# Performance work log

Measured on AMD Instinct MI355X. Metric: run time of the kernel, lower is better.

The kernel has to match this reference:

```python
import jax, jax.numpy as jnp
import numpy as np

HEADS = 16
TARGET_TOKENS = 128  # deterministic choice of image_tokens (original picks randomly from [729,128])


def _1d_sincos(embed_dim, pos):
    omega = np.arange(embed_dim // 2, dtype=np.float32)
    omega /= embed_dim / 2.0
    omega = 1.0 / 10000 ** omega
    out = np.einsum('m,d->md', pos.reshape(-1), omega)
    return np.concatenate([np.sin(out), np.cos(out)], axis=1)


def spatial_pos_embed(embed_dim, grid_size):
    d_sp = embed_dim // 4 * 3
    gh = np.arange(grid_size, dtype=np.float32)
    grid = np.stack(np.meshgrid(gh, gh), axis=0).reshape([2, 1, grid_size, grid_size])
    emb = np.concatenate([_1d_sincos(d_sp // 2, grid[0]), _1d_sincos(d_sp // 2, grid[1])], axis=1)
    emb = emb[np.newaxis]
    pad = np.zeros((1, emb.shape[1], embed_dim - d_sp), dtype=np.float32)
    return np.concatenate([pad, emb], axis=-1).reshape(1, grid_size * grid_size, embed_dim)


def setup_inputs() -> dict:
    key = jax.random.key(0)
    ks = jax.random.split(key, 4)
    B, P, C, H = 64, 729, 1152, 3584
    x = jax.random.normal(ks[0], (B, P, C), jnp.float32)
    w1 = jax.random.normal(ks[1], (C, H), jnp.float32) * (1.0 / np.sqrt(C))
    b1 = jnp.zeros((H,), jnp.float32)
    w2 = jax.random.normal(ks[2], (H, H), jnp.float32) * (1.0 / np.sqrt(H))
    b2 = jnp.zeros((H,), jnp.float32)
    spatial_pos = jnp.asarray(spatial_pos_embed(C, 27))
    return {'x': x, 'spatial_pos': spatial_pos, 'w1': w1, 'b1': b1,
            'w2': w2, 'b2': b2, 'local_num_frames': 1}


def _match_indices(metric, r):
    # ToMe bipartite soft matching: metric [B, T, d]
    metric = metric / jnp.linalg.norm(metric, axis=-1, keepdims=True)
    a, b = metric[:, ::2], metric[:, 1::2]
    scores = jnp.einsum('bic,bjc->bij', a, b)   # [B, Ta, Tb]
    node_max = scores.max(-1)
    node_idx = scores.argmax(-1)
    edge_idx = jnp.argsort(-node_max, axis=-1)
    unm_idx = edge_idx[:, r:]                    # kept src tokens
    src_idx = edge_idx[:, :r]                    # merged src tokens
    dst_idx = jnp.take_along_axis(node_idx, src_idx, axis=-1)
    return unm_idx, src_idx, dst_idx


def _merge_sum(x, unm_idx, src_idx, dst_idx):
    src, dst = x[:, ::2], x[:, 1::2]
    unm = jnp.take_along_axis(src, unm_idx[:, :, None], axis=1)
    sel = jnp.take_along_axis(src, src_idx[:, :, None], axis=1)
    dst = jax.vmap(lambda d, i, v: d.at[i].add(v))(dst, dst_idx, sel)
    return jnp.concatenate([unm, dst], axis=1)


def merge_tokens(x, target, heads):
    b, p, c = x.shape
    if p == target:
        return x
    rs, tmp = [], p
    while tmp != target:
        if tmp - target <= tmp // 2:
            rs.append(tmp - target)
            break
        rs.append(tmp // 2)
        tmp -= tmp // 2
    size = jnp.ones((b, p, 1), x.dtype)
    for r in rs:  # static schedule, e.g. [364, 182, 55]
        t = x.shape[1]
        metric = x.reshape(b, t, heads, c // heads).mean(2)
        idxs = _match_indices(metric, r)
        x = _merge_sum(x * size, *idxs)
        size = _merge_sum(size, *idxs)
        x = x / size
    return x


def reference(x, spatial_pos, w1, b1, w2, b2, local_num_frames):
    # is_image=True path
    x = x + spatial_pos
    x = merge_tokens(x, TARGET_TOKENS, HEADS)
    h = jax.nn.gelu(jnp.einsum('bpc,ch->bph', x, w1) + b1, approximate=False)
    return jnp.einsum('bph,ho->bpo', h, w2) + b2
```

## Files before the change

kernel.cpp:

```cpp
#include <hip/hip_runtime.h>
#include <hip/hip_bf16.h>
#include <stdint.h>

#define BB 64
#define P0 729
#define CC 1152
#define HD 72
#define NHEAD 16
#define HH 3584
#define TT 128
#define NSTR 365
#define SCB 384
#define MAXCB 6

typedef __hip_bfloat16 bf16;
typedef unsigned short u16;
typedef __attribute__((ext_vector_type(8))) short short8;
typedef __attribute__((ext_vector_type(4))) float floatx4;

__device__ inline u16 f2bf(float v) {
  bf16 h = __float2bfloat16(v);
  return *(u16*)&h;
}

__device__ inline void load_lds16(const void* g, void* l) {
  __builtin_amdgcn_global_load_lds(
      (const __attribute__((address_space(1))) uint32_t*)g,
      (__attribute__((address_space(3))) uint32_t*)l, 16, 0, 0);
}

__global__ __launch_bounds__(128)
void k_init(const float* __restrict__ x, const float* __restrict__ pos,
            double* __restrict__ mo, int* __restrict__ amap) {
  __shared__ float xs[CC], ps[CC];
  int bp = blockIdx.x;
  int p = bp % P0;
  int tid = threadIdx.x;
  const float4* xr = (const float4*)(x + (size_t)bp * CC);
  const float4* pr = (const float4*)(pos + (size_t)p * CC);
  for (int idx = tid; idx < CC / 4; idx += 128) {
    ((float4*)xs)[idx] = xr[idx];
    ((float4*)ps)[idx] = pr[idx];
  }
  __syncthreads();
  if (tid < HD) {
    double s = 0.0;
    #pragma unroll
    for (int h = 0; h < NHEAD; ++h) {
      int c = h * HD + tid;
      s += (double)xs[c] + (double)ps[c];
    }
    mo[(size_t)bp * HD + tid] = s * (1.0 / 16.0);
  }
  if (tid == 0) amap[bp] = p;
}

__global__ void k_rnorm(const double* __restrict__ m, double* __restrict__ rn, int t) {
  int bi = blockIdx.x;
  int lane = threadIdx.x;
  const double* row = m + (size_t)bi * HD;
  double v = 0.0;
  if (lane < HD) { double a = row[lane]; v = a * a; }
  if (lane < HD - 64) { double a = row[lane + 64]; v += a * a; }
  for (int off = 32; off; off >>= 1) v += __shfl_down(v, off, 64);
  if (lane == 0) {
    int b = bi / t, i = bi % t;
    rn[b * P0 + i] = 1.0 / sqrt(v);
  }
}

__global__ __launch_bounds__(256)
void k_score2(const double* __restrict__ m, const double* __restrict__ rn,
              double* __restrict__ pmax, int* __restrict__ pidx,
              int t, int s, int d) {
  __shared__ double sL[64][37];
  __shared__ double sD[64][37];
  int b = blockIdx.z;
  int i0 = blockIdx.x * 64, j0 = blockIdx.y * 64;
  int tid = threadIdx.x;
  int tx = tid & 15, ty = tid >> 4;
  double acc[4][4] = {};
  for (int kc = 0; kc < HD; kc += 36) {
    for (int idx = tid; idx < 64 * 36; idx += 256) {
      int row = idx / 36, k = idx - row * 36;
      int i = i0 + row;
      sL[row][k] = (i < s) ? m[((size_t)b * t + 2 * i) * HD + kc + k] : 0.0;
      int j = j0 + row;
      sD[row][k] = (j < d) ? m[((size_t)b * t + 2 * j + 1) * HD + kc + k] : 0.0;
    }
    __syncthreads();
    #pragma unroll 6
    for (int k = 0; k < 36; ++k) {
      double la[4], ld[4];
      #pragma unroll
      for (int a = 0; a < 4; ++a) la[a] = sL[ty + 16 * a][k];
      #pragma unroll
      for (int c = 0; c < 4; ++c) ld[c] = sD[tx + 16 * c][k];
      #pragma unroll
      for (int a = 0; a < 4; ++a)
        #pragma unroll
        for (int c = 0; c < 4; ++c)
          acc[a][c] += la[a] * ld[c];
    }
    __syncthreads();
  }
  #pragma unroll
  for (int a = 0; a < 4; ++a) {
    int i = i0 + ty + 16 * a;
    double rni = (i < s) ? rn[b * P0 + 2 * i] : 0.0;
    double best = -1e300; int bj = 0x7fffffff;
    #pragma unroll
    for (int c = 0; c < 4; ++c) {
      int j = j0 + tx + 16 * c;
      double sc = (j < d) ? acc[a][c] * rni * rn[b * P0 + 2 * j + 1] : -1e300;
      if (sc > best) { best = sc; bj = j; }
    }
    for (int off = 8; off; off >>= 1) {
      double ov = __shfl_down(best, off, 16);
      int oj = __shfl_down(bj, off, 16);
      if (ov > best || (ov == best && oj < bj)) { best = ov; bj = oj; }
    }
    if (tx == 0 && i < s) {
      pmax[((size_t)b * MAXCB + blockIdx.y) * SCB + i] = best;
      pidx[((size_t)b * MAXCB + blockIdx.y) * SCB + i] = bj;
    }
  }
}

__global__ void k_colred(const double* __restrict__ pmax, const int* __restrict__ pidx,
                         double* __restrict__ nmax, int* __restrict__ nidx,
                         int s, int ncb) {
  int b = blockIdx.x, i = threadIdx.x;
  if (i >= s) return;
  double best = -1e300; int bj = 0x7fffffff;
  for (int cb = 0; cb < ncb; ++cb) {
    double v = pmax[((size_t)b * MAXCB + cb) * SCB + i];
    int j = pidx[((size_t)b * MAXCB + cb) * SCB + i];
    if (v > best) { best = v; bj = j; }
  }
  nmax[b * NSTR + i] = best; nidx[b * NSTR + i] = bj;
}

template <int SZ>
__global__ __launch_bounds__(512)
void k_sort(const double* __restrict__ nmax, int* __restrict__ eidx, int s) {
  __shared__ double v[SZ];
  __shared__ int ix[SZ];
  int b = blockIdx.x, tid = threadIdx.x;
  if (tid < s) { v[tid] = nmax[b * NSTR + tid]; ix[tid] = tid; }
  else { v[tid] = -1e308; ix[tid] = 1024 + tid; }
  __syncthreads();
  for (int k = 2; k <= SZ; k <<= 1)
    for (int j = k >> 1; j > 0; j >>= 1) {
      int l = tid ^ j;
      if (l > tid) {
        double va = v[tid], vb = v[l]; int ia = ix[tid], ib = ix[l];
        bool b_before_a = (vb > va) || (vb == va && ib < ia);
        bool a_before_b = (va > vb) || (va == vb && ia < ib);
        bool dir = ((tid & k) == 0);
        bool sw = dir ? b_before_a : a_before_b;
        if (sw) { v[tid] = vb; v[l] = va; ix[tid] = ib; ix[l] = ia; }
      }
      __syncthreads();
    }
  if (tid < s) eidx[b * NSTR + tid] = ix[tid];
}

__global__ __launch_bounds__(512)
void k_mapround(const int* __restrict__ eidx, const int* __restrict__ nidx,
                int* __restrict__ amap, int t, int s, int r, int unm) {
  __shared__ int pos_of[NSTR];
  __shared__ int rmap[P0];
  int b = blockIdx.x, tid = threadIdx.x;
  for (int q = tid; q < s; q += 512) pos_of[eidx[b * NSTR + q]] = q;
  __syncthreads();
  for (int j = tid; j < t; j += 512) {
    int nm;
    if (j & 1) {
      nm = unm + (j >> 1);
    } else {
      int i = j >> 1;
      int q = pos_of[i];
      nm = (q >= r) ? (q - r)
                    : (unm + nidx[b * NSTR + i]);
    }
    rmap[j] = nm;
  }
  __syncthreads();
  for (int p = tid; p < P0; p += 512) {
    int cur = amap[b * P0 + p];
    amap[b * P0 + p] = rmap[cur];
  }
}

__global__ void k_gather_d(const double* __restrict__ mo, double* __restrict__ mn,
                           const int* __restrict__ eidx,
                           int t, int r, int unm, int tnew) {
  size_t idx = (size_t)blockIdx.x * 256 + threadIdx.x;
  size_t total = (size_t)BB * tnew * HD;
  if (idx >= total) return;
  int k = idx % HD;
  int o = (idx / HD) % tnew;
  int b = idx / ((size_t)HD * tnew);
  int tok = (o < unm) ? 2 * eidx[b * NSTR + r + o] : 2 * (o - unm) + 1;
  mn[idx] = mo[((size_t)b * t + tok) * HD + k];
}

__global__ void k_scatter_d(const double* __restrict__ mo, double* __restrict__ mn,
                            const int* __restrict__ eidx, const int* __restrict__ nidx,
                            int t, int r, int unm, int tnew) {
  size_t idx = (size_t)blockIdx.x * 256 + threadIdx.x;
  size_t total = (size_t)BB * r * HD;
  if (idx >= total) return;
  int k = idx % HD;
  int q = (idx / HD) % r;
  int b = idx / ((size_t)HD * r);
  int si = eidx[b * NSTR + q];
  int di = nidx[b * NSTR + si];
  atomicAdd(&mn[((size_t)b * tnew + unm + di) * HD + k],
            mo[((size_t)b * t + 2 * si) * HD + k]);
}

__global__ __launch_bounds__(256)
void k_buildcsr(const int* __restrict__ amap, int* __restrict__ sizes,
                int* __restrict__ offs, int* __restrict__ list) {
  __shared__ int cnt[TT], off_s[TT], cur[TT];
  int b = blockIdx.x, tid = threadIdx.x;
  if (tid < TT) { cnt[tid] = 0; cur[tid] = 0; }
  __syncthreads();
  for (int p = tid; p < P0; p += 256) atomicAdd(&cnt[amap[b * P0 + p]], 1);
  __syncthreads();
  if (tid == 0) {
    int acc = 0;
    for (int o = 0; o < TT; ++o) { off_s[o] = acc; acc += cnt[o]; }
  }
  __syncthreads();
  if (tid < TT) { sizes[b * TT + tid] = cnt[tid]; offs[b * TT + tid] = off_s[tid]; }
  for (int p = tid; p < P0; p += 256) {
    int o = amap[b * P0 + p];
    int pos = atomicAdd(&cur[o], 1);
    list[b * P0 + off_s[o] + pos] = p;
  }
}

__global__ __launch_bounds__(256)
void k_assemble(const float* __restrict__ x, const float* __restrict__ pos,
                const int* __restrict__ sizes, const int* __restrict__ offs,
                const int* __restrict__ list, bf16* __restrict__ xb) {
  int o = blockIdx.x, b = blockIdx.y, tid = threadIdx.x;
  int n = sizes[b * TT + o];
  int off = offs[b * TT + o];
  const int C4 = CC / 4;
  float4 a0 = {0.f, 0.f, 0.f, 0.f}, a1 = {0.f, 0.f, 0.f, 0.f};
  for (int i = 0; i < n; ++i) {
    int p = list[b * P0 + off + i];
    const float4* xr = (const float4*)(x + ((size_t)b * P0 + p) * CC);
    const float4* pr = (const float4*)(pos + (size_t)p * CC);
    float4 v = xr[tid], w = pr[tid];
    a0.x += v.x + w.x; a0.y += v.y + w.y; a0.z += v.z + w.z; a0.w += v.w + w.w;
    if (tid < C4 - 256) {
      float4 v1 = xr[tid + 256], w1 = pr[tid + 256];
      a1.x += v1.x + w1.x; a1.y += v1.y + w1.y; a1.z += v1.z + w1.z; a1.w += v1.w + w1.w;
    }
  }
  float inv = 1.0f / (float)n;
  bf16* orow = xb + ((size_t)b * TT + o) * CC;
  ushort4 pk;
  pk.x = f2bf(a0.x * inv);
  pk.y = f2bf(a0.y * inv);
  pk.z = f2bf(a0.z * inv);
  pk.w = f2bf(a0.w * inv);
  ((ushort4*)orow)[tid] = pk;
  if (tid < C4 - 256) {
    ushort4 pk1;
    pk1.x = f2bf(a1.x * inv);
    pk1.y = f2bf(a1.y * inv);
    pk1.z = f2bf(a1.z * inv);
    pk1.w = f2bf(a1.w * inv);
    ((ushort4*)orow)[tid + 256] = pk1;
  }
}

__global__ void k_transpose(const float* __restrict__ w, bf16* __restrict__ wt,
                            int K, int N) {
  __shared__ float tile[32][33];
  int n0 = blockIdx.x * 32, k0 = blockIdx.y * 32;
  int tx = threadIdx.x, ty = threadIdx.y;
  #pragma unroll
  for (int yy = 0; yy < 32; yy += 8)
    tile[ty + yy][tx] = w[(size_t)(k0 + ty + yy) * N + n0 + tx];
  __syncthreads();
  #pragma unroll
  for (int yy = 0; yy < 32; yy += 8)
    wt[(size_t)(n0 + ty + yy) * K + k0 + tx] = __float2bfloat16(tile[tx][ty + yy]);
}


#define SBAR __builtin_amdgcn_sched_barrier(0)

#define STAGE_A(BUF, HHF, KT) do {                                        \
    int ktc_ = (KT) < nkt ? (KT) : nkt - 1;                               \
    const u16* s_ = gA + (size_t)(HHF) * 128 * K + ktc_ * 64;             \
    u16* d_ = dA + (BUF) * 16384 + (HHF) * 8192;                          \
    load_lds16(s_, d_);                                                   \
    load_lds16(s_ + (size_t)64 * K, d_ + 4096);                           \
  } while (0)

#define STAGE_B(BUF, HHF, KT) do {                                        \
    int ktc_ = (KT) < nkt ? (KT) : nkt - 1;                               \
    const u16* s_ = gB + (size_t)(HHF) * 128 * K + ktc_ * 64;             \
    u16* d_ = dB + (BUF) * 16384 + (HHF) * 8192;                          \
    load_lds16(s_, d_);                                                   \
    load_lds16(s_ + (size_t)64 * K, d_ + 4096);                           \
  } while (0)

#define LOADA(QA) do {                                                    \
    _Pragma("unroll")                                                     \
    for (int f_ = 0; f_ < 4; ++f_) {                                      \
      const u16* p_ = Ab + ((QA) * 128 + wr64 + f_ * 16 + lrow) * 64;     \
      af[f_][0] = *(const short8*)(p_ + swo0);                            \
      af[f_][1] = *(const short8*)(p_ + swo1);                            \
    }                                                                     \
  } while (0)

#define LOADB(QB) do {                                                    \
    _Pragma("unroll")                                                     \
    for (int g_ = 0; g_ < 2; ++g_) {                                      \
      const u16* p_ = Bb + ((QB) * 128 + wc32 + g_ * 16 + lrow) * 64;     \
      bfr[g_][0] = *(const short8*)(p_ + swo0);                           \
      bfr[g_][1] = *(const short8*)(p_ + swo1);                           \
    }                                                                     \
  } while (0)

#define DO_MFMA(QA, QB) do {                                              \
    _Pragma("unroll")                                                     \
    for (int ks_ = 0; ks_ < 2; ++ks_)                                     \
      _Pragma("unroll")                                                   \
      for (int f_ = 0; f_ < 4; ++f_)                                      \
        _Pragma("unroll")                                                 \
        for (int g_ = 0; g_ < 2; ++g_)                                    \
          acc[QA][QB][f_][g_] = __builtin_amdgcn_mfma_f32_16x16x32_bf16(  \
              af[f_][ks_], bfr[g_][ks_], acc[QA][QB][f_][g_], 0, 0, 0);   \
  } while (0)

#define MIDBAR() do {                                                     \
    SBAR;                                                                 \
    __builtin_amdgcn_s_barrier();                                         \
    asm volatile("s_waitcnt lgkmcnt(0)" ::: "memory");                    \
    SBAR;                                                                 \
    __builtin_amdgcn_s_setprio(1);                                        \
  } while (0)

#define ENDBAR() do {                                                     \
    __builtin_amdgcn_s_setprio(0);                                        \
    SBAR;                                                                 \
    __builtin_amdgcn_s_barrier();                                         \
    SBAR;                                                                 \
  } while (0)

#define ENDBAR_VM() do {                                                  \
    __builtin_amdgcn_s_setprio(0);                                        \
    SBAR;                                                                 \
    asm volatile("s_waitcnt vmcnt(6)" ::: "memory");                      \
    SBAR;                                                                 \
    __builtin_amdgcn_s_barrier();                                         \
    SBAR;                                                                 \
  } while (0)

template <int EPI>
__global__ __launch_bounds__(512, 2)
void k_gemm(const u16* __restrict__ A, const u16* __restrict__ Bt,
            const float* __restrict__ bias, void* __restrict__ Cout,
            int M, int N, int K) {
  __shared__ u16 sAall[32768];
  __shared__ u16 sBall[32768];
  (void)M;
  const int tid = threadIdx.x;
  const int m0 = blockIdx.y * 256, n0 = blockIdx.x * 256;
  const int wave = tid >> 6, lane = tid & 63;
  const int wr64 = (wave >> 2) * 64;
  const int wc32 = (wave & 3) * 32;
  const int quad = lane >> 4, lrow = lane & 15;
  const int sw = lrow & 7;
  const int swo0 = ((quad ^ sw)) << 3;
  const int swo1 = (((quad | 4) ^ sw)) << 3;
  const int nkt = K >> 6;

  const int r = tid >> 3;
  const int c16 = (tid & 7) ^ (r & 7);
  const u16* gA = A + (size_t)(m0 + r) * K + c16 * 8;
  const u16* gB = Bt + (size_t)(n0 + r) * K + c16 * 8;
  u16* dA = sAall + (tid << 3);
  u16* dB = sBall + (tid << 3);

  floatx4 acc[2][2][4][2] = {};
  short8 af[4][2], bfr[2][2];

  STAGE_A(0, 0, 0); STAGE_B(0, 1, 0); STAGE_A(0, 1, 0); STAGE_B(0, 0, 0);
  STAGE_A(1, 0, 1); STAGE_B(1, 1, 1); STAGE_A(1, 1, 1);
  SBAR;
  asm volatile("s_waitcnt vmcnt(6)" ::: "memory");
  SBAR;
  __builtin_amdgcn_s_barrier();
  SBAR;

  for (int t = 0; t < nkt; ++t) {
    const int bb = t & 1;
    const u16* Ab = sAall + bb * 16384;
    const u16* Bb = sBall + bb * 16384;
    LOADA(0); LOADB(0);
    STAGE_B(bb ^ 1, 0, t + 1);
    MIDBAR(); DO_MFMA(0, 0); ENDBAR();
    LOADB(1);
    STAGE_A(bb, 0, t + 2);
    MIDBAR(); DO_MFMA(0, 1); ENDBAR();
    LOADA(1);
    STAGE_B(bb, 1, t + 2);
    MIDBAR(); DO_MFMA(1, 1); ENDBAR();
    LOADB(0);
    STAGE_A(bb, 1, t + 2);
    MIDBAR(); DO_MFMA(1, 0); ENDBAR_VM();
  }

  #pragma unroll
  for (int qb = 0; qb < 2; ++qb)
    #pragma unroll
    for (int g = 0; g < 2; ++g) {
      int col = n0 + qb * 128 + wc32 + g * 16 + lrow;
      float bc = bias[col];
      #pragma unroll
      for (int qa = 0; qa < 2; ++qa)
        #pragma unroll
        for (int f = 0; f < 4; ++f)
          #pragma unroll
          for (int rg = 0; rg < 4; ++rg) {
            int row = m0 + qa * 128 + wr64 + f * 16 + quad * 4 + rg;
            float v = acc[qa][qb][f][g][rg] + bc;
            if (EPI == 0) {
              float gl = 0.5f * v * (1.0f + erff(v * 0.70710678118654752f));
              ((bf16*)Cout)[(size_t)row * N + col] = __float2bfloat16(gl);
            } else {
              ((float*)Cout)[(size_t)row * N + col] = v;
            }
          }
    }
}

extern "C" void kernel_launch(void* const* d_in, const int* in_sizes, int n_in,
                              void* d_out, int out_size, void* d_ws, size_t ws_size,
                              hipStream_t stream) {
  const float* x   = (const float*)d_in[0];
  const float* pos = (const float*)d_in[1];
  const float* w1  = (const float*)d_in[2];
  const float* b1  = (const float*)d_in[3];
  const float* w2  = (const float*)d_in[4];
  const float* b2  = (const float*)d_in[5];

  uint8_t* wsp = (uint8_t*)d_ws;
  size_t off = 0;
  auto alloc = [&](size_t bytes) -> void* {
    void* p = wsp + off;
    off += (bytes + 255) & ~(size_t)255;
    return p;
  };
  double* m_a  = (double*)alloc((size_t)BB * P0 * HD * 8);
  double* m_b  = (double*)alloc((size_t)BB * NSTR * HD * 8);
  double* rn   = (double*)alloc((size_t)BB * P0 * 8);
  double* nmax = (double*)alloc((size_t)BB * NSTR * 8);
  int*    nidx = (int*)alloc((size_t)BB * NSTR * 4);
  int*    eidx = (int*)alloc((size_t)BB * NSTR * 4);
  double* pmax = (double*)alloc((size_t)BB * MAXCB * SCB * 8);
  int*    pidx = (int*)alloc((size_t)BB * MAXCB * SCB * 4);
  int*    amap = (int*)alloc((size_t)BB * P0 * 4);
  int*    szs  = (int*)alloc((size_t)BB * TT * 4);
  int*    offs = (int*)alloc((size_t)BB * TT * 4);
  int*    list = (int*)alloc((size_t)BB * P0 * 4);
  bf16*   xb   = (bf16*)alloc((size_t)BB * TT * CC * 2);
  bf16*   w1t  = (bf16*)alloc((size_t)HH * CC * 2);
  bf16*   w2t  = (bf16*)alloc((size_t)HH * HH * 2);
  bf16*   hb   = (bf16*)alloc((size_t)BB * TT * HH * 2);

  k_init<<<BB * P0, 128, 0, stream>>>(x, pos, m_a, amap);
  dim3 tb(32, 8);
  k_transpose<<<dim3(HH / 32, CC / 32), tb, 0, stream>>>(w1, w1t, CC, HH);
  k_transpose<<<dim3(HH / 32, HH / 32), tb, 0, stream>>>(w2, w2t, HH, HH);

  struct Rnd { int t, s, d, r, unm, tnew; };
  const Rnd R[3] = {{729, 365, 364, 364, 1, 365},
                    {365, 183, 182, 182, 1, 183},
                    {183,  92,  91,  55, 37, 128}};
  double* msrc[3] = {m_a, m_b, m_a};
  double* mdst[3] = {m_b, m_a, m_b};

  for (int rr = 0; rr < 3; ++rr) {
    Rnd q = R[rr];
    k_rnorm<<<BB * q.t, 64, 0, stream>>>(msrc[rr], rn, q.t);
    int rt = (q.s + 63) / 64, ct = (q.d + 63) / 64;
    dim3 sg(rt, ct, BB);
    k_score2<<<sg, 256, 0, stream>>>(msrc[rr], rn, pmax, pidx, q.t, q.s, q.d);
    k_colred<<<BB, 512, 0, stream>>>(pmax, pidx, nmax, nidx, q.s, ct);
    if (rr == 0)      k_sort<512><<<BB, 512, 0, stream>>>(nmax, eidx, q.s);
    else if (rr == 1) k_sort<256><<<BB, 256, 0, stream>>>(nmax, eidx, q.s);
    else              k_sort<128><<<BB, 128, 0, stream>>>(nmax, eidx, q.s);
    k_mapround<<<BB, 512, 0, stream>>>(eidx, nidx, amap, q.t, q.s, q.r, q.unm);
    if (rr < 2) {
      size_t tg = (size_t)BB * q.tnew * HD;
      k_gather_d<<<(tg + 255) / 256, 256, 0, stream>>>(msrc[rr], mdst[rr], eidx, q.t, q.r, q.unm, q.tnew);
      size_t ts = (size_t)BB * q.r * HD;
      k_scatter_d<<<(ts + 255) / 256, 256, 0, stream>>>(msrc[rr], mdst[rr], eidx, nidx, q.t, q.r, q.unm, q.tnew);
    }
  }

  k_buildcsr<<<BB, 256, 0, stream>>>(amap, szs, offs, list);
  k_assemble<<<dim3(TT, BB), 256, 0, stream>>>(x, pos, szs, offs, list, xb);

  k_gemm<0><<<dim3(HH / 256, (BB * TT) / 256), 512, 0, stream>>>(
      (const u16*)xb, (const u16*)w1t, b1, hb, BB * TT, HH, CC);
  k_gemm<1><<<dim3(HH / 256, (BB * TT) / 256), 512, 0, stream>>>(
      (const u16*)hb, (const u16*)w2t, b2, d_out, BB * TT, HH, HH);
}
```

Before: 1.404 ms.

## Replace CSR gather assembly with atomic row scatter into float accumulator

```diff
diff --git a/kernel.cpp b/kernel.cpp
--- a/kernel.cpp
+++ b/kernel.cpp
@@ -222,62 +222,76 @@
 }
 
 __global__ __launch_bounds__(256)
-void k_buildcsr(const int* __restrict__ amap, int* __restrict__ sizes,
-                int* __restrict__ offs, int* __restrict__ list) {
-  __shared__ int cnt[TT], off_s[TT], cur[TT];
+void k_sizes(const int* __restrict__ amap, int* __restrict__ sizes) {
+  __shared__ int cnt[TT];
   int b = blockIdx.x, tid = threadIdx.x;
-  if (tid < TT) { cnt[tid] = 0; cur[tid] = 0; }
+  if (tid < TT) cnt[tid] = 0;
   __syncthreads();
   for (int p = tid; p < P0; p += 256) atomicAdd(&cnt[amap[b * P0 + p]], 1);
   __syncthreads();
-  if (tid == 0) {
-    int acc = 0;
-    for (int o = 0; o < TT; ++o) { off_s[o] = acc; acc += cnt[o]; }
-  }
-  __syncthreads();
-  if (tid < TT) { sizes[b * TT + tid] = cnt[tid]; offs[b * TT + tid] = off_s[tid]; }
-  for (int p = tid; p < P0; p += 256) {
-    int o = amap[b * P0 + p];
-    int pos = atomicAdd(&cur[o], 1);
-    list[b * P0 + off_s[o] + pos] = p;
-  }
+  if (tid < TT) sizes[b * TT + tid] = cnt[tid];
 }
 
 __global__ __launch_bounds__(256)
-void k_assemble(const float* __restrict__ x, const float* __restrict__ pos,
-                const int* __restrict__ sizes, const int* __restrict__ offs,
-                const int* __restrict__ list, bf16* __restrict__ xb) {
-  int o = blockIdx.x, b = blockIdx.y, tid = threadIdx.x;
-  int n = sizes[b * TT + o];
-  int off = offs[b * TT + o];
-  const int C4 = CC / 4;
-  float4 a0 = {0.f, 0.f, 0.f, 0.f}, a1 = {0.f, 0.f, 0.f, 0.f};
-  for (int i = 0; i < n; ++i) {
-    int p = list[b * P0 + off + i];
-    const float4* xr = (const float4*)(x + ((size_t)b * P0 + p) * CC);
-    const float4* pr = (const float4*)(pos + (size_t)p * CC);
-    float4 v = xr[tid], w = pr[tid];
-    a0.x += v.x + w.x; a0.y += v.y + w.y; a0.z += v.z + w.z; a0.w += v.w + w.w;
-    if (tid < C4 - 256) {
-      float4 v1 = xr[tid + 256], w1 = pr[tid + 256];
-      a1.x += v1.x + w1.x; a1.y += v1.y + w1.y; a1.z += v1.z + w1.z; a1.w += v1.w + w1.w;
-    }
-  }
-  float inv = 1.0f / (float)n;
-  bf16* orow = xb + ((size_t)b * TT + o) * CC;
-  ushort4 pk;
-  pk.x = f2bf(a0.x * inv);
-  pk.y = f2bf(a0.y * inv);
-  pk.z = f2bf(a0.z * inv);
-  pk.w = f2bf(a0.w * inv);
-  ((ushort4*)orow)[tid] = pk;
-  if (tid < C4 - 256) {
-    ushort4 pk1;
-    pk1.x = f2bf(a1.x * inv);
-    pk1.y = f2bf(a1.y * inv);
-    pk1.z = f2bf(a1.z * inv);
-    pk1.w = f2bf(a1.w * inv);
-    ((ushort4*)orow)[tid + 256] = pk1;
+void k_clear(float4* __restrict__ a, int n4) {
+  int stride = gridDim.x * 256;
+  for (int i = blockIdx.x * 256 + threadIdx.x; i < n4; i += stride)
+    a[i] = make_float4(0.f, 0.f, 0.f, 0.f);
+}
+
+__global__ __launch_bounds__(256)
+void k_scatter_rows(const float* __restrict__ x, const float* __restrict__ pos,
+                    const int* __restrict__ amap, float* __restrict__ accum) {
+  int w = threadIdx.x >> 6, lane = threadIdx.x & 63;
+  int bp = blockIdx.x * 4 + w;
+  int b = bp / P0, p = bp - b * P0;
+  int o = amap[bp];
+  const float4* xr = (const float4*)(x + (size_t)bp * CC);
+  const float4* pr = (const float4*)(pos + (size_t)p * CC);
+  float* arow = accum + ((size_t)b * TT + o) * CC;
+  #pragma unroll
+  for (int t = 0; t < 4; ++t) {
+    int idx = lane + t * 64;
+    float4 v = xr[idx], q = pr[idx];
+    atomicAdd(&arow[4 * idx + 0], v.x + q.x);
+    atomicAdd(&arow[4 * idx + 1], v.y + q.y);
+    atomicAdd(&arow[4 * idx + 2], v.z + q.z);
+    atomicAdd(&arow[4 * idx + 3], v.w + q.w);
+  }
+  if (lane < 32) {
+    int idx = lane + 256;
+    float4 v = xr[idx], q = pr[idx];
+    atomicAdd(&arow[4 * idx + 0], v.x + q.x);
+    atomicAdd(&arow[4 * idx + 1], v.y + q.y);
+    atomicAdd(&arow[4 * idx + 2], v.z + q.z);
+    atomicAdd(&arow[4 * idx + 3], v.w + q.w);
+  }
+}
+
+__global__ __launch_bounds__(256)
+void k_normalize(const float* __restrict__ accum, const int* __restrict__ szs,
+                 bf16* __restrict__ xb) {
+  int w = threadIdx.x >> 6, lane = threadIdx.x & 63;
+  int row = blockIdx.x * 4 + w;
+  float inv = 1.0f / (float)szs[row];
+  const float4* ar = (const float4*)(accum + (size_t)row * CC);
+  ushort4* orow = (ushort4*)(xb + (size_t)row * CC);
+  #pragma unroll
+  for (int t = 0; t < 4; ++t) {
+    int idx = lane + t * 64;
+    float4 v = ar[idx];
+    ushort4 pk;
+    pk.x = f2bf(v.x * inv); pk.y = f2bf(v.y * inv);
+    pk.z = f2bf(v.z * inv); pk.w = f2bf(v.w * inv);
+    orow[idx] = pk;
+  }
+  if (lane < 32) {
+    int idx = lane + 256;
+    float4 v = ar[idx];
+    ushort4 pk;
+    pk.x = f2bf(v.x * inv); pk.y = f2bf(v.y * inv);
+    pk.z = f2bf(v.z * inv); pk.w = f2bf(v.w * inv);
+    orow[idx] = pk;
   }
 }
 
@@ -473,12 +487,12 @@
   int*    pidx = (int*)alloc((size_t)BB * MAXCB * SCB * 4);
   int*    amap = (int*)alloc((size_t)BB * P0 * 4);
   int*    szs  = (int*)alloc((size_t)BB * TT * 4);
-  int*    offs = (int*)alloc((size_t)BB * TT * 4);
-  int*    list = (int*)alloc((size_t)BB * P0 * 4);
   bf16*   xb   = (bf16*)alloc((size_t)BB * TT * CC * 2);
   bf16*   w1t  = (bf16*)alloc((size_t)HH * CC * 2);
   bf16*   w2t  = (bf16*)alloc((size_t)HH * HH * 2);
   bf16*   hb   = (bf16*)alloc((size_t)BB * TT * HH * 2);
+
+  float* accum = (float*)m_a;
 
   k_init<<<BB * P0, 128, 0, stream>>>(x, pos, m_a, amap);
   dim3 tb(32, 8);
@@ -511,8 +525,10 @@
     }
   }
 
-  k_buildcsr<<<BB, 256, 0, stream>>>(amap, szs, offs, list);
-  k_assemble<<<dim3(TT, BB), 256, 0, stream>>>(x, pos, szs, offs, list, xb);
+  k_sizes<<<BB, 256, 0, stream>>>(amap, szs);
+  k_clear<<<4096, 256, 0, stream>>>((float4*)accum, BB * TT * CC / 4);
+  k_scatter_rows<<<(BB * P0) / 4, 256, 0, stream>>>(x, pos, amap, accum);
+  k_normalize<<<(BB * TT) / 4, 256, 0, stream>>>(accum, szs, xb);
 
   k_gemm<0><<<dim3(HH / 256, (BB * TT) / 256), 512, 0, stream>>>(
       (const u16*)xb, (const u16*)w1t, b1, hb, BB * TT, HH, CC);
```

New measurement: 2.123 ms. 51.2% more time.
